# Kernel optimization log

Hardware: AMD Instinct MI355X
Metric: run time of the kernel (lower is better)

## Reference

```python
import jax, jax.numpy as jnp
import numpy as np

HEADS = 16
LN_EPS = 1e-12
MINUS_INF = -10000.0  # matches DeepSpeed's minus_inf constant


def setup_inputs() -> dict:
    key = jax.random.key(0)
    ks = jax.random.split(key, 6)
    B, S, H = 2, 2048, 2048
    x = jax.random.normal(ks[0], (B, S, H), dtype=jnp.float32)
    mask = jnp.zeros((B, 1, 1, S), dtype=jnp.float32)  # additive float mask (no padding)
    qkvw = jax.random.normal(ks[1], (H, 3 * H), dtype=jnp.float32) * 0.02
    qkvb = jax.random.normal(ks[2], (3 * H,), dtype=jnp.float32) * 0.02
    ow = jax.random.normal(ks[3], (H, H), dtype=jnp.float32) * 0.02
    norm_w = jnp.ones((H,), dtype=jnp.float32)
    norm_b = jnp.zeros((H,), dtype=jnp.float32)
    return {"x": x, "mask": mask, "qkvw": qkvw, "qkvb": qkvb, "ow": ow,
            "norm_w": norm_w, "norm_b": norm_b}


def _layernorm(x, g, b):
    mu = jnp.mean(x, axis=-1, keepdims=True)
    var = jnp.mean(jnp.square(x - mu), axis=-1, keepdims=True)
    return (x - mu) * jax.lax.rsqrt(var + LN_EPS) * g + b


def reference(x, mask, qkvw, qkvb, ow, norm_w, norm_b):
    B, S, H = x.shape
    dh = H // HEADS
    # QKVGemmOp: fused layernorm + QKV projection
    inp_norm = _layernorm(x, norm_w, norm_b)                      # [B,S,H]
    qkv = jnp.einsum('bsh,he->bse', inp_norm, qkvw) + qkvb        # [B,S,3H]
    q, k, v = jnp.split(qkv, 3, axis=-1)
    q = q.reshape(B, S, HEADS, dh).transpose(0, 2, 1, 3)          # [B,Hd,S,dh]
    k = k.reshape(B, S, HEADS, dh).transpose(0, 2, 1, 3)
    v = v.reshape(B, S, HEADS, dh).transpose(0, 2, 1, 3)
    # SoftmaxContextOp: kernel scales q and k each by 1/norm_factor,
    # norm_factor = d_head**0.25 (use_mup=False) -> net scale 1/sqrt(d_head)
    scale = 1.0 / jnp.sqrt(jnp.asarray(dh, dtype=x.dtype))
    scores = jnp.einsum('bhqd,bhkd->bhqk', q, k) * scale          # [B,Hd,S,S]
    causal = jnp.tril(jnp.ones((S, S), dtype=bool))
    scores = jnp.where(causal[None, None], scores + mask, MINUS_INF)
    probs = jax.nn.softmax(scores, axis=-1)
    ctx = jnp.einsum('bhqk,bhkd->bhqd', probs, v)                 # [B,Hd,S,dh]
    ctx = ctx.transpose(0, 2, 1, 3).reshape(B, S, H)
    # VectorMatMulOp: output projection (no bias here)
    out = jnp.einsum('bsh,ho->bso', ctx, ow)                      # [B,S,H]
    return (out, k, v, ctx, inp_norm)
```

## Files before the change

### kernel.cpp

```cpp
#include <hip/hip_runtime.h>

typedef short bf16x8 __attribute__((ext_vector_type(8)));
typedef float floatx4 __attribute__((ext_vector_type(4)));

#define MFMA16(a, b, c) __builtin_amdgcn_mfma_f32_16x16x32_bf16((a), (b), (c), 0, 0, 0)

__device__ __forceinline__ unsigned short f2bf(float f) {
    union { float f; unsigned int u; } v; v.f = f;
    unsigned int u = v.u;
    return (unsigned short)((u + 0x7FFFu + ((u >> 16) & 1u)) >> 16);
}

__device__ __forceinline__ void gld_lds16(const void* g, void* l) {
    __builtin_amdgcn_global_load_lds(
        (const __attribute__((address_space(1))) unsigned int*)g,
        (__attribute__((address_space(3))) unsigned int*)l, 16, 0, 0);
}

__global__ __launch_bounds__(256) void ln_kernel(
        const float* __restrict__ x, const float* __restrict__ g,
        const float* __restrict__ be, float* __restrict__ yo,
        unsigned short* __restrict__ yb) {
    int row = blockIdx.x, t = threadIdx.x;
    const float* xr = x + (size_t)row * 2048;
    float4 a = ((const float4*)xr)[2 * t];
    float4 b = ((const float4*)xr)[2 * t + 1];
    float s = a.x + a.y + a.z + a.w + b.x + b.y + b.z + b.w;
    float q = a.x * a.x + a.y * a.y + a.z * a.z + a.w * a.w +
              b.x * b.x + b.y * b.y + b.z * b.z + b.w * b.w;
    for (int m = 1; m < 64; m <<= 1) { s += __shfl_xor(s, m); q += __shfl_xor(q, m); }
    __shared__ float red[8];
    if ((t & 63) == 0) { red[t >> 6] = s; red[4 + (t >> 6)] = q; }
    __syncthreads();
    s = red[0] + red[1] + red[2] + red[3];
    q = red[4] + red[5] + red[6] + red[7];
    float mean = s * (1.0f / 2048.0f);
    float var = q * (1.0f / 2048.0f) - mean * mean;
    float rs = rsqrtf(var + 1e-12f);
    float4 g0 = ((const float4*)g)[2 * t], g1 = ((const float4*)g)[2 * t + 1];
    float4 b0 = ((const float4*)be)[2 * t], b1 = ((const float4*)be)[2 * t + 1];
    float4 y0, y1;
    y0.x = (a.x - mean) * rs * g0.x + b0.x;
    y0.y = (a.y - mean) * rs * g0.y + b0.y;
    y0.z = (a.z - mean) * rs * g0.z + b0.z;
    y0.w = (a.w - mean) * rs * g0.w + b0.w;
    y1.x = (b.x - mean) * rs * g1.x + b1.x;
    y1.y = (b.y - mean) * rs * g1.y + b1.y;
    y1.z = (b.z - mean) * rs * g1.z + b1.z;
    y1.w = (b.w - mean) * rs * g1.w + b1.w;
    float* yr = yo + (size_t)row * 2048;
    ((float4*)yr)[2 * t] = y0;
    ((float4*)yr)[2 * t + 1] = y1;
    union { unsigned short u[8]; uint4 v; } pk;
    pk.u[0] = f2bf(y0.x); pk.u[1] = f2bf(y0.y); pk.u[2] = f2bf(y0.z); pk.u[3] = f2bf(y0.w);
    pk.u[4] = f2bf(y1.x); pk.u[5] = f2bf(y1.y); pk.u[6] = f2bf(y1.z); pk.u[7] = f2bf(y1.w);
    *(uint4*)(yb + (size_t)row * 2048 + t * 8) = pk.v;
}

__global__ __launch_bounds__(256) void transpose_cvt(
        const float* __restrict__ src, unsigned short* __restrict__ dst,
        int K, int N) {
    __shared__ unsigned short tile[64][73];
    int n0 = blockIdx.x * 64, k0 = blockIdx.y * 64;
    size_t bo = (size_t)blockIdx.z * K * N;
    int t = threadIdx.x;
    for (int p = 0; p < 4; p++) {
        int idx = p * 256 + t; int r = idx >> 4; int c = (idx & 15) * 4;
        float4 v = *(const float4*)(src + bo + (size_t)(k0 + r) * N + n0 + c);
        tile[r][c] = f2bf(v.x); tile[r][c + 1] = f2bf(v.y);
        tile[r][c + 2] = f2bf(v.z); tile[r][c + 3] = f2bf(v.w);
    }
    __syncthreads();
    for (int p = 0; p < 4; p++) {
        int idx = p * 256 + t; int n = idx >> 4; int c = (idx & 15) * 4;
        ushort4 o;
        o.x = tile[c][n]; o.y = tile[c + 1][n];
        o.z = tile[c + 2][n]; o.w = tile[c + 3][n];
        *(ushort4*)(dst + bo + (size_t)(n0 + n) * K + k0 + c) = o;
    }
}

#define NT_QKV 32

__device__ __forceinline__ void stage_A(const unsigned short* __restrict__ Ag,
        unsigned short* As, int mh, int m0, int kt, int tid) {
#pragma unroll
    for (int j = 0; j < 2; j++) {
        int G = j * 512 + tid;
        int s = (G >> 3) & 63;
        int gr = G & 7;
        int row = j * 128 + mh * 64 + s;
        const unsigned short* src =
            Ag + (size_t)(m0 + row) * 2048 + kt * 64 + ((gr ^ (s & 7)) << 3);
        unsigned short* dst = As + j * 8192 + mh * 4096 + (tid >> 6) * 512;
        gld_lds16(src, dst);
    }
}

__device__ __forceinline__ void stage_B(const unsigned short* __restrict__ Bg,
        unsigned short* Bs, int nh, int n0, int kt, int tid) {
#pragma unroll
    for (int j = 0; j < 2; j++) {
        int G = j * 512 + tid;
        int wcc = G >> 8;
        int s = (G >> 3) & 31;
        int gr = G & 7;
        int row = wcc * 64 + nh * 32 + s;
        const unsigned short* src =
            Bg + (size_t)(n0 + row) * 2048 + kt * 64 + ((gr ^ (s & 7)) << 3);
        unsigned short* dst = Bs + wcc * 4096 + nh * 2048 + ((tid >> 6) & 3) * 512;
        gld_lds16(src, dst);
    }
}

__device__ __forceinline__ bf16x8 ldfrag(const unsigned short* S, int row, int ks,
                                         int quad, int ln15) {
    int gr = ((ks << 2) | quad) ^ (ln15 & 7);
    return *(const bf16x8*)(S + row * 64 + gr * 8);
}

#define PHASE_SYNC()                                        \
    __builtin_amdgcn_s_barrier();                           \
    asm volatile("s_waitcnt lgkmcnt(0)" ::: "memory");      \
    __builtin_amdgcn_sched_barrier(0);                      \
    __builtin_amdgcn_s_setprio(1)

#define PHASE_END()                                         \
    __builtin_amdgcn_s_setprio(0);                          \
    asm volatile("s_waitcnt vmcnt(4)" ::: "memory");        \
    __builtin_amdgcn_s_barrier()

__device__ __forceinline__ void qkv_tile(
        const unsigned short* __restrict__ Ag, const unsigned short* __restrict__ Bg,
        unsigned short* Asc, unsigned short* Bsc,
        unsigned short* Asn, unsigned short* Bsn,
        int t, int m0, int n0, int tid, int wr, int wc, int ln15, int quad,
        floatx4 (&acc)[8][4]) {
    bf16x8 a[4][2], bb[2][2];
    bool pf = (t + 1 < NT_QKV);
#pragma unroll
    for (int m = 0; m < 4; m++) {
        a[m][0] = ldfrag(Asc, wr * 128 + m * 16 + ln15, 0, quad, ln15);
        a[m][1] = ldfrag(Asc, wr * 128 + m * 16 + ln15, 1, quad, ln15);
    }
#pragma unroll
    for (int n = 0; n < 2; n++) {
        bb[n][0] = ldfrag(Bsc, wc * 64 + n * 16 + ln15, 0, quad, ln15);
        bb[n][1] = ldfrag(Bsc, wc * 64 + n * 16 + ln15, 1, quad, ln15);
    }
    if (pf) stage_B(Bg, Bsn, 0, n0, t + 1, tid);
    PHASE_SYNC();
#pragma unroll
    for (int m = 0; m < 4; m++)
#pragma unroll
        for (int n = 0; n < 2; n++) {
            acc[m][n] = MFMA16(a[m][0], bb[n][0], acc[m][n]);
            acc[m][n] = MFMA16(a[m][1], bb[n][1], acc[m][n]);
        }
    PHASE_END();
#pragma unroll
    for (int n = 0; n < 2; n++) {
        bb[n][0] = ldfrag(Bsc, wc * 64 + (2 + n) * 16 + ln15, 0, quad, ln15);
        bb[n][1] = ldfrag(Bsc, wc * 64 + (2 + n) * 16 + ln15, 1, quad, ln15);
    }
    if (pf) stage_A(Ag, Asn, 0, m0, t + 1, tid);
    PHASE_SYNC();
#pragma unroll
    for (int m = 0; m < 4; m++)
#pragma unroll
        for (int n = 0; n < 2; n++) {
            acc[m][2 + n] = MFMA16(a[m][0], bb[n][0], acc[m][2 + n]);
            acc[m][2 + n] = MFMA16(a[m][1], bb[n][1], acc[m][2 + n]);
        }
    PHASE_END();
#pragma unroll
    for (int m = 0; m < 4; m++) {
        a[m][0] = ldfrag(Asc, wr * 128 + (4 + m) * 16 + ln15, 0, quad, ln15);
        a[m][1] = ldfrag(Asc, wr * 128 + (4 + m) * 16 + ln15, 1, quad, ln15);
    }
    if (pf) stage_B(Bg, Bsn, 1, n0, t + 1, tid);
    PHASE_SYNC();
#pragma unroll
    for (int m = 0; m < 4; m++)
#pragma unroll
        for (int n = 0; n < 2; n++) {
            acc[4 + m][2 + n] = MFMA16(a[m][0], bb[n][0], acc[4 + m][2 + n]);
            acc[4 + m][2 + n] = MFMA16(a[m][1], bb[n][1], acc[4 + m][2 + n]);
        }
    PHASE_END();
#pragma unroll
    for (int n = 0; n < 2; n++) {
        bb[n][0] = ldfrag(Bsc, wc * 64 + n * 16 + ln15, 0, quad, ln15);
        bb[n][1] = ldfrag(Bsc, wc * 64 + n * 16 + ln15, 1, quad, ln15);
    }
    if (pf) stage_A(Ag, Asn, 1, m0, t + 1, tid);
    PHASE_SYNC();
#pragma unroll
    for (int m = 0; m < 4; m++)
#pragma unroll
        for (int n = 0; n < 2; n++) {
            acc[4 + m][n] = MFMA16(a[m][0], bb[n][0], acc[4 + m][n]);
            acc[4 + m][n] = MFMA16(a[m][1], bb[n][1], acc[4 + m][n]);
        }
    PHASE_END();
}

__global__ __launch_bounds__(512, 2) void gemm_qkv(
        const unsigned short* __restrict__ A, const unsigned short* __restrict__ Bt,
        const float* __restrict__ bias, float* __restrict__ ko,
        float* __restrict__ vo, unsigned short* __restrict__ qws,
        unsigned short* __restrict__ kbf) {
    __shared__ __align__(16) unsigned short As[2][16384];
    __shared__ __align__(16) unsigned short Bs[2][16384];
    int bid = blockIdx.x;
    int xcd = bid & 7, idx = bid >> 3;
    int mt = (xcd & 3) * 4 + idx / 12;
    int ntile = (xcd >> 2) * 12 + idx % 12;
    int m0 = mt * 256, n0 = ntile * 256;
    int tid = threadIdx.x;
    int wave = tid >> 6, lane = tid & 63, ln15 = lane & 15, quad = lane >> 4;
    int wr = wave >> 2, wc = wave & 3;
    floatx4 acc[8][4] = {};
    stage_B(Bt, Bs[0], 0, n0, 0, tid);
    stage_A(A, As[0], 0, m0, 0, tid);
    stage_B(Bt, Bs[0], 1, n0, 0, tid);
    stage_A(A, As[0], 1, m0, 0, tid);
    asm volatile("s_waitcnt vmcnt(4)" ::: "memory");
    __builtin_amdgcn_s_barrier();
#pragma unroll 1
    for (int t = 0; t < NT_QKV; t += 2) {
        qkv_tile(A, Bt, As[0], Bs[0], As[1], Bs[1], t,     m0, n0, tid, wr, wc, ln15, quad, acc);
        qkv_tile(A, Bt, As[1], Bs[1], As[0], Bs[0], t + 1, m0, n0, tid, wr, wc, ln15, quad, acc);
    }
#pragma unroll
    for (int mi = 0; mi < 8; mi++) {
        int row = m0 + wr * 128 + mi * 16 + quad * 4;
#pragma unroll
        for (int ni = 0; ni < 4; ni++) {
            int col = n0 + wc * 64 + ni * 16 + ln15;
            float bv = bias[col];
#pragma unroll
            for (int r = 0; r < 4; r++) {
                float val = acc[mi][ni][r] + bv;
                int rr = row + r;
                int b = rr >> 11, s = rr & 2047;
                if (col < 2048) {
                    qws[(size_t)rr * 2048 + col] = f2bf(val);
                } else if (col < 4096) {
                    int cc = col - 2048; int h = cc >> 7, d = cc & 127;
                    size_t o = ((size_t)(b * 16 + h) * 2048 + s) * 128 + d;
                    ko[o] = val;
                    kbf[o] = f2bf(val);
                } else {
                    int cc = col - 4096; int h = cc >> 7, d = cc & 127;
                    vo[((size_t)(b * 16 + h) * 2048 + s) * 128 + d] = val;
                }
            }
        }
    }
}

__global__ __launch_bounds__(256) void gemm_out(
        const float* __restrict__ Actx, const unsigned short* __restrict__ Bt,
        float* __restrict__ out) {
    __shared__ unsigned short As[128 * 72];
    __shared__ unsigned short Bs[128 * 72];
    int m0 = blockIdx.y * 128, n0 = blockIdx.x * 128;
    int t = threadIdx.x;
    int wave = t >> 6, lane = t & 63, ln15 = lane & 15, quad = lane >> 4;
    int wm = wave >> 1, wn = wave & 1;
    floatx4 acc[4][4] = {};
    for (int k0 = 0; k0 < 2048; k0 += 64) {
        for (int p = 0; p < 4; p++) {
            int idx = p * 256 + t; int r = idx >> 3; int c = (idx & 7) * 8;
            const float* ap = Actx + (size_t)(m0 + r) * 2048 + k0 + c;
            float4 u0 = ((const float4*)ap)[0], u1 = ((const float4*)ap)[1];
            union { unsigned short u[8]; uint4 v; } pk;
            pk.u[0] = f2bf(u0.x); pk.u[1] = f2bf(u0.y); pk.u[2] = f2bf(u0.z); pk.u[3] = f2bf(u0.w);
            pk.u[4] = f2bf(u1.x); pk.u[5] = f2bf(u1.y); pk.u[6] = f2bf(u1.z); pk.u[7] = f2bf(u1.w);
            *(uint4*)&As[r * 72 + c] = pk.v;
            *(uint4*)&Bs[r * 72 + c] = *(const uint4*)(Bt + (size_t)(n0 + r) * 2048 + k0 + c);
        }
        __syncthreads();
        for (int ks = 0; ks < 2; ks++) {
            bf16x8 af[4], bfr[4];
            for (int i = 0; i < 4; i++)
                af[i] = *(const bf16x8*)&As[(wm * 64 + i * 16 + ln15) * 72 + ks * 32 + quad * 8];
            for (int i = 0; i < 4; i++)
                bfr[i] = *(const bf16x8*)&Bs[(wn * 64 + i * 16 + ln15) * 72 + ks * 32 + quad * 8];
            for (int mi = 0; mi < 4; mi++)
                for (int ni = 0; ni < 4; ni++)
                    acc[mi][ni] = MFMA16(af[mi], bfr[ni], acc[mi][ni]);
        }
        __syncthreads();
    }
    for (int mi = 0; mi < 4; mi++) {
        int row = m0 + wm * 64 + mi * 16 + quad * 4;
        for (int ni = 0; ni < 4; ni++) {
            int col = n0 + wn * 64 + ni * 16 + ln15;
            for (int r = 0; r < 4; r++)
                out[(size_t)(row + r) * 2048 + col] = acc[mi][ni][r];
        }
    }
}

__device__ __forceinline__ void stage_kv(const unsigned short* __restrict__ kb,
                                         const unsigned short* __restrict__ vTb,
                                         int c0, int tid,
                                         unsigned short* KsB, unsigned short* VtB) {
    int wb = (tid >> 6) << 6;
#pragma unroll
    for (int i = 0; i < 4; i++) {
        int p = i * 256 + tid;
        int r = p >> 4, s = p & 15;
        int g = s ^ (r & 7);
        gld_lds16(kb + (size_t)(c0 + r) * 128 + g * 8, KsB + (i * 256 + wb) * 8);
    }
#pragma unroll
    for (int i = 0; i < 4; i++) {
        int p = i * 256 + tid;
        int d = p >> 3, s = p & 7;
        int g = s ^ (d & 7);
        gld_lds16(vTb + (size_t)d * 2048 + c0 + g * 8, VtB + (i * 256 + wb) * 8);
    }
}

__global__ __launch_bounds__(256, 2) void attn_kernel(
        const unsigned short* __restrict__ qws, const unsigned short* __restrict__ kbf,
        const unsigned short* __restrict__ vT, const float* __restrict__ mask,
        float* __restrict__ ctxo) {
    __shared__ __align__(16) unsigned short Ks[2][64 * 128];
    __shared__ __align__(16) unsigned short Vt[2][128 * 64];
    __shared__ unsigned short Pl[4 * 16 * 72];
    int jp = blockIdx.x, h = blockIdx.y, b = blockIdx.z;
    int t = threadIdx.x, wave = t >> 6, lane = t & 63, ln15 = lane & 15, quad = lane >> 4;
    int x7 = ln15 & 7;
    const float scale = 0.08838834764831845f;

    const unsigned short* kb = kbf + (size_t)(b * 16 + h) * 2048 * 128;
    const unsigned short* vTb = vT + (size_t)(b * 16 + h) * 128 * 2048;
    const float* mb = mask + (size_t)b * 2048;

    int cur = 0;
    stage_kv(kb, vTb, 0, t, Ks[0], Vt[0]);

#pragma unroll 1
    for (int half = 0; half < 2; half++) {
        int qt = half ? (31 - jp) : jp;
        int Q0 = qt * 64;

        bf16x8 qf[4];
        const unsigned short* qbase =
            qws + ((size_t)(b * 2048 + Q0 + wave * 16 + ln15)) * 2048 + h * 128;
#pragma unroll
        for (int ks = 0; ks < 4; ks++)
            qf[ks] = *(const bf16x8*)(qbase + ks * 32 + quad * 8);

        float m_r[4], l_r[4];
        floatx4 o[8] = {};
#pragma unroll
        for (int r = 0; r < 4; r++) { m_r[r] = -1e30f; l_r[r] = 0.0f; }

        int nkt = qt + 1;
#pragma unroll 1
        for (int kt = 0; kt < nkt; kt++) {
            int c0 = kt * 64;
            bool hn = true; int nc0 = 0;
            if (kt + 1 < nkt)      nc0 = c0 + 64;
            else if (half == 0)    nc0 = 0;
            else                   hn = false;
            if (hn) {
                stage_kv(kb, vTb, nc0, t, Ks[cur ^ 1], Vt[cur ^ 1]);
                asm volatile("s_waitcnt vmcnt(8)" ::: "memory");
            } else {
                asm volatile("s_waitcnt vmcnt(0)" ::: "memory");
            }
            __builtin_amdgcn_s_barrier();
            const unsigned short* KsB = Ks[cur];
            const unsigned short* VtB = Vt[cur];

            floatx4 cs[4] = {};
            __builtin_amdgcn_s_setprio(1);
#pragma unroll
            for (int ks = 0; ks < 4; ks++)
#pragma unroll
                for (int ni = 0; ni < 4; ni++) {
                    int rr = ni * 16 + ln15;
                    int sl = (ks * 4 + quad) ^ x7;
                    bf16x8 kfr = *(const bf16x8*)&KsB[rr * 128 + sl * 8];
                    cs[ni] = MFMA16(qf[ks], kfr, cs[ni]);
                }
            __builtin_amdgcn_s_setprio(0);

            float sv[4][4];
            float mt[4] = {-1e30f, -1e30f, -1e30f, -1e30f};
            if (kt == qt) {
#pragma unroll
                for (int ni = 0; ni < 4; ni++) {
                    int cg = c0 + ni * 16 + ln15;
                    float mk = mb[cg];
#pragma unroll
                    for (int r = 0; r < 4; r++) {
                        int qg = Q0 + wave * 16 + quad * 4 + r;
                        float v = (cg <= qg) ? fmaf(cs[ni][r], scale, mk) : -10000.0f;
                        sv[ni][r] = v;
                        mt[r] = fmaxf(mt[r], v);
                    }
                }
            } else {
#pragma unroll
                for (int ni = 0; ni < 4; ni++) {
                    float mk = mb[c0 + ni * 16 + ln15];
#pragma unroll
                    for (int r = 0; r < 4; r++) {
                        float v = fmaf(cs[ni][r], scale, mk);
                        sv[ni][r] = v;
                        mt[r] = fmaxf(mt[r], v);
                    }
                }
            }
#pragma unroll
            for (int m = 1; m < 16; m <<= 1)
#pragma unroll
                for (int r = 0; r < 4; r++) mt[r] = fmaxf(mt[r], __shfl_xor(mt[r], m));

            bool grow = false;
#pragma unroll
            for (int r = 0; r < 4; r++) grow = grow || (mt[r] > m_r[r] + 8.0f);
            if (__any((int)grow)) {
#pragma unroll
                for (int r = 0; r < 4; r++) {
                    float mn = fmaxf(m_r[r], mt[r]);
                    float al = __expf(m_r[r] - mn);
                    m_r[r] = mn;
                    l_r[r] *= al;
#pragma unroll
                    for (int nj = 0; nj < 8; nj++) o[nj][r] *= al;
                }
            }

            float lt[4] = {0.0f, 0.0f, 0.0f, 0.0f};
#pragma unroll
            for (int ni = 0; ni < 4; ni++)
#pragma unroll
                for (int r = 0; r < 4; r++) {
                    float p = __expf(sv[ni][r] - m_r[r]);
                    sv[ni][r] = p;
                    lt[r] += p;
                }
#pragma unroll
            for (int m = 1; m < 16; m <<= 1)
#pragma unroll
                for (int r = 0; r < 4; r++) lt[r] += __shfl_xor(lt[r], m);
#pragma unroll
            for (int r = 0; r < 4; r++) l_r[r] += lt[r];

            unsigned short* pw = &Pl[wave * 16 * 72];
#pragma unroll
            for (int ni = 0; ni < 4; ni++)
#pragma unroll
                for (int r = 0; r < 4; r++)
                    pw[(quad * 4 + r) * 72 + ni * 16 + ln15] = f2bf(sv[ni][r]);

            __builtin_amdgcn_s_setprio(1);
#pragma unroll
            for (int ks2 = 0; ks2 < 2; ks2++) {
                bf16x8 pf = *(const bf16x8*)&Pl[(wave * 16 + ln15) * 72 + ks2 * 32 + quad * 8];
#pragma unroll
                for (int nj = 0; nj < 8; nj++) {
                    int dd = nj * 16 + ln15;
                    int sl = (ks2 * 4 + quad) ^ x7;
                    bf16x8 vf = *(const bf16x8*)&VtB[dd * 64 + sl * 8];
                    o[nj] = MFMA16(pf, vf, o[nj]);
                }
            }
            __builtin_amdgcn_s_setprio(0);
            __builtin_amdgcn_s_barrier();
            cur ^= 1;
        }

        float rl[4];
#pragma unroll
        for (int r = 0; r < 4; r++) rl[r] = 1.0f / l_r[r];
#pragma unroll
        for (int nj = 0; nj < 8; nj++)
#pragma unroll
            for (int r = 0; r < 4; r++) {
                int s = Q0 + wave * 16 + quad * 4 + r;
                ctxo[((size_t)(b * 2048 + s)) * 2048 + h * 128 + nj * 16 + ln15] = o[nj][r] * rl[r];
            }
    }
}

extern "C" void kernel_launch(void* const* d_in, const int* in_sizes, int n_in,
                              void* d_out, int out_size, void* d_ws, size_t ws_size,
                              hipStream_t stream) {
    const float* x      = (const float*)d_in[0];
    const float* mask   = (const float*)d_in[1];
    const float* qkvw   = (const float*)d_in[2];
    const float* qkvb   = (const float*)d_in[3];
    const float* ow     = (const float*)d_in[4];
    const float* norm_w = (const float*)d_in[5];
    const float* norm_b = (const float*)d_in[6];

    float* out      = (float*)d_out;
    float* k_out    = out + 8388608;
    float* v_out    = out + 16777216;
    float* ctx_out  = out + 25165824;
    float* norm_out = out + 33554432;

    unsigned short* ws    = (unsigned short*)d_ws;
    unsigned short* xn    = ws;
    unsigned short* qkvwT = ws + 8388608;
    unsigned short* owT   = ws + 8388608 + 12582912;
    unsigned short* qws   = owT + 4194304;
    unsigned short* vT    = qws + 8388608;
    unsigned short* kbf   = vT + 8388608;

    ln_kernel<<<4096, 256, 0, stream>>>(x, norm_w, norm_b, norm_out, xn);
    transpose_cvt<<<dim3(96, 32, 1), 256, 0, stream>>>(qkvw, qkvwT, 2048, 6144);
    transpose_cvt<<<dim3(32, 32, 1), 256, 0, stream>>>(ow, owT, 2048, 2048);
    gemm_qkv<<<dim3(384), 512, 0, stream>>>(xn, qkvwT, qkvb, k_out, v_out, qws, kbf);
    transpose_cvt<<<dim3(2, 32, 32), 256, 0, stream>>>(v_out, vT, 2048, 128);
    attn_kernel<<<dim3(16, 16, 2), 256, 0, stream>>>(qws, kbf, vT, mask, ctx_out);
    gemm_out<<<dim3(16, 32), 256, 0, stream>>>(ctx_out, owT, out);
}
```

Measured before the change: 550.6 us.

## Fuse prep kernels, emit bf16 ctx from attention, async-load gemm_out tiles

Merges layernorm and both weight transpose-converts into one launch. The attention kernel now also writes a bf16 copy of ctx into the freed xn workspace, so gemm_out no longer reads fp32 ctx and converts it per tile. gemm_out loads A and B straight into LDS with global_load_lds, uses an unpadded 64-stride layout, and remaps blocks for XCD locality. This trades extra bf16 stores in attention and possible LDS bank conflicts from dropping the padding for less conversion work and fewer launches.

After: 542.6 us. Within noise of the previous version (-1.4%).

```diff
diff --git a/kernel.cpp b/kernel.cpp
--- a/kernel.cpp
+++ b/kernel.cpp
@@ -17,44 +17,75 @@
         (__attribute__((address_space(3))) unsigned int*)l, 16, 0, 0);
 }
 
-__global__ __launch_bounds__(256) void ln_kernel(
+__global__ __launch_bounds__(256) void prep_kernel(
         const float* __restrict__ x, const float* __restrict__ g,
         const float* __restrict__ be, float* __restrict__ yo,
-        unsigned short* __restrict__ yb) {
-    int row = blockIdx.x, t = threadIdx.x;
-    const float* xr = x + (size_t)row * 2048;
-    float4 a = ((const float4*)xr)[2 * t];
-    float4 b = ((const float4*)xr)[2 * t + 1];
-    float s = a.x + a.y + a.z + a.w + b.x + b.y + b.z + b.w;
-    float q = a.x * a.x + a.y * a.y + a.z * a.z + a.w * a.w +
-              b.x * b.x + b.y * b.y + b.z * b.z + b.w * b.w;
-    for (int m = 1; m < 64; m <<= 1) { s += __shfl_xor(s, m); q += __shfl_xor(q, m); }
+        unsigned short* __restrict__ yb,
+        const float* __restrict__ qkvw, unsigned short* __restrict__ qkvwT,
+        const float* __restrict__ ow, unsigned short* __restrict__ owT) {
     __shared__ float red[8];
-    if ((t & 63) == 0) { red[t >> 6] = s; red[4 + (t >> 6)] = q; }
+    __shared__ unsigned short tile[64][73];
+    int bid = blockIdx.x, t = threadIdx.x;
+    if (bid < 4096) {
+        int row = bid;
+        const float* xr = x + (size_t)row * 2048;
+        float4 a = ((const float4*)xr)[2 * t];
+        float4 b = ((const float4*)xr)[2 * t + 1];
+        float s = a.x + a.y + a.z + a.w + b.x + b.y + b.z + b.w;
+        float q = a.x * a.x + a.y * a.y + a.z * a.z + a.w * a.w +
+                  b.x * b.x + b.y * b.y + b.z * b.z + b.w * b.w;
+        for (int m = 1; m < 64; m <<= 1) { s += __shfl_xor(s, m); q += __shfl_xor(q, m); }
+        if ((t & 63) == 0) { red[t >> 6] = s; red[4 + (t >> 6)] = q; }
+        __syncthreads();
+        s = red[0] + red[1] + red[2] + red[3];
+        q = red[4] + red[5] + red[6] + red[7];
+        float mean = s * (1.0f / 2048.0f);
+        float var = q * (1.0f / 2048.0f) - mean * mean;
+        float rs = rsqrtf(var + 1e-12f);
+        float4 g0 = ((const float4*)g)[2 * t], g1 = ((const float4*)g)[2 * t + 1];
+        float4 b0 = ((const float4*)be)[2 * t], b1 = ((const float4*)be)[2 * t + 1];
+        float4 y0, y1;
+        y0.x = (a.x - mean) * rs * g0.x + b0.x;
+        y0.y = (a.y - mean) * rs * g0.y + b0.y;
+        y0.z = (a.z - mean) * rs * g0.z + b0.z;
+        y0.w = (a.w - mean) * rs * g0.w + b0.w;
+        y1.x = (b.x - mean) * rs * g1.x + b1.x;
+        y1.y = (b.y - mean) * rs * g1.y + b1.y;
+        y1.z = (b.z - mean) * rs * g1.z + b1.z;
+        y1.w = (b.w - mean) * rs * g1.w + b1.w;
+        float* yr = yo + (size_t)row * 2048;
+        ((float4*)yr)[2 * t] = y0;
+        ((float4*)yr)[2 * t + 1] = y1;
+        union { unsigned short u[8]; uint4 v; } pk;
+        pk.u[0] = f2bf(y0.x); pk.u[1] = f2bf(y0.y); pk.u[2] = f2bf(y0.z); pk.u[3] = f2bf(y0.w);
+        pk.u[4] = f2bf(y1.x); pk.u[5] = f2bf(y1.y); pk.u[6] = f2bf(y1.z); pk.u[7] = f2bf(y1.w);
+        *(uint4*)(yb + (size_t)row * 2048 + t * 8) = pk.v;
+        return;
+    }
+    const float* src; unsigned short* dst; int N, n0, k0;
+    if (bid < 4096 + 3072) {
+        int b2 = bid - 4096;
+        src = qkvw; dst = qkvwT; N = 6144;
+        n0 = (b2 % 96) * 64; k0 = (b2 / 96) * 64;
+    } else {
+        int b3 = bid - 7168;
+        src = ow; dst = owT; N = 2048;
+        n0 = (b3 % 32) * 64; k0 = (b3 / 32) * 64;
+    }
+    for (int p = 0; p < 4; p++) {
+        int idx = p * 256 + t; int r = idx >> 4; int c = (idx & 15) * 4;
+        float4 v = *(const float4*)(src + (size_t)(k0 + r) * N + n0 + c);
+        tile[r][c] = f2bf(v.x); tile[r][c + 1] = f2bf(v.y);
+        tile[r][c + 2] = f2bf(v.z); tile[r][c + 3] = f2bf(v.w);
+    }
     __syncthreads();
-    s = red[0] + red[1] + red[2] + red[3];
-    q = red[4] + red[5] + red[6] + red[7];
-    float mean = s * (1.0f / 2048.0f);
-    float var = q * (1.0f / 2048.0f) - mean * mean;
-    float rs = rsqrtf(var + 1e-12f);
-    float4 g0 = ((const float4*)g)[2 * t], g1 = ((const float4*)g)[2 * t + 1];
-    float4 b0 = ((const float4*)be)[2 * t], b1 = ((const float4*)be)[2 * t + 1];
-    float4 y0, y1;
-    y0.x = (a.x - mean) * rs * g0.x + b0.x;
-    y0.y = (a.y - mean) * rs * g0.y + b0.y;
-    y0.z = (a.z - mean) * rs * g0.z + b0.z;
-    y0.w = (a.w - mean) * rs * g0.w + b0.w;
-    y1.x = (b.x - mean) * rs * g1.x + b1.x;
-    y1.y = (b.y - mean) * rs * g1.y + b1.y;
-    y1.z = (b.z - mean) * rs * g1.z + b1.z;
-    y1.w = (b.w - mean) * rs * g1.w + b1.w;
-    float* yr = yo + (size_t)row * 2048;
-    ((float4*)yr)[2 * t] = y0;
-    ((float4*)yr)[2 * t + 1] = y1;
-    union { unsigned short u[8]; uint4 v; } pk;
-    pk.u[0] = f2bf(y0.x); pk.u[1] = f2bf(y0.y); pk.u[2] = f2bf(y0.z); pk.u[3] = f2bf(y0.w);
-    pk.u[4] = f2bf(y1.x); pk.u[5] = f2bf(y1.y); pk.u[6] = f2bf(y1.z); pk.u[7] = f2bf(y1.w);
-    *(uint4*)(yb + (size_t)row * 2048 + t * 8) = pk.v;
+    for (int p = 0; p < 4; p++) {
+        int idx = p * 256 + t; int n = idx >> 4; int c = (idx & 15) * 4;
+        ushort4 o;
+        o.x = tile[c][n]; o.y = tile[c + 1][n];
+        o.z = tile[c + 2][n]; o.w = tile[c + 3][n];
+        *(ushort4*)(dst + (size_t)(n0 + n) * 2048 + k0 + c) = o;
+    }
 }
 
 __global__ __launch_bounds__(256) void transpose_cvt(
@@ -261,33 +292,32 @@
 }
 
 __global__ __launch_bounds__(256) void gemm_out(
-        const float* __restrict__ Actx, const unsigned short* __restrict__ Bt,
+        const unsigned short* __restrict__ Ab, const unsigned short* __restrict__ Bt,
         float* __restrict__ out) {
-    __shared__ unsigned short As[128 * 72];
-    __shared__ unsigned short Bs[128 * 72];
-    int m0 = blockIdx.y * 128, n0 = blockIdx.x * 128;
+    __shared__ unsigned short As[128 * 64];
+    __shared__ unsigned short Bs[128 * 64];
+    int bid = blockIdx.x;
+    int xcd = bid & 7, idx = bid >> 3;
+    int mt = (xcd & 3) * 8 + (idx >> 3);
+    int nt = (xcd >> 2) * 8 + (idx & 7);
+    int m0 = mt * 128, n0 = nt * 128;
     int t = threadIdx.x;
     int wave = t >> 6, lane = t & 63, ln15 = lane & 15, quad = lane >> 4;
     int wm = wave >> 1, wn = wave & 1;
     floatx4 acc[4][4] = {};
     for (int k0 = 0; k0 < 2048; k0 += 64) {
         for (int p = 0; p < 4; p++) {
-            int idx = p * 256 + t; int r = idx >> 3; int c = (idx & 7) * 8;
-            const float* ap = Actx + (size_t)(m0 + r) * 2048 + k0 + c;
-            float4 u0 = ((const float4*)ap)[0], u1 = ((const float4*)ap)[1];
-            union { unsigned short u[8]; uint4 v; } pk;
-            pk.u[0] = f2bf(u0.x); pk.u[1] = f2bf(u0.y); pk.u[2] = f2bf(u0.z); pk.u[3] = f2bf(u0.w);
-            pk.u[4] = f2bf(u1.x); pk.u[5] = f2bf(u1.y); pk.u[6] = f2bf(u1.z); pk.u[7] = f2bf(u1.w);
-            *(uint4*)&As[r * 72 + c] = pk.v;
-            *(uint4*)&Bs[r * 72 + c] = *(const uint4*)(Bt + (size_t)(n0 + r) * 2048 + k0 + c);
+            int ix = p * 256 + t; int r = ix >> 3; int c = (ix & 7) * 8;
+            gld_lds16(Ab + (size_t)(m0 + r) * 2048 + k0 + c, As + p * 2048 + wave * 512);
+            gld_lds16(Bt + (size_t)(n0 + r) * 2048 + k0 + c, Bs + p * 2048 + wave * 512);
         }
         __syncthreads();
         for (int ks = 0; ks < 2; ks++) {
             bf16x8 af[4], bfr[4];
             for (int i = 0; i < 4; i++)
-                af[i] = *(const bf16x8*)&As[(wm * 64 + i * 16 + ln15) * 72 + ks * 32 + quad * 8];
+                af[i] = *(const bf16x8*)&As[(wm * 64 + i * 16 + ln15) * 64 + ks * 32 + quad * 8];
             for (int i = 0; i < 4; i++)
-                bfr[i] = *(const bf16x8*)&Bs[(wn * 64 + i * 16 + ln15) * 72 + ks * 32 + quad * 8];
+                bfr[i] = *(const bf16x8*)&Bs[(wn * 64 + i * 16 + ln15) * 64 + ks * 32 + quad * 8];
             for (int mi = 0; mi < 4; mi++)
                 for (int ni = 0; ni < 4; ni++)
                     acc[mi][ni] = MFMA16(af[mi], bfr[ni], acc[mi][ni]);
@@ -328,7 +358,7 @@
 __global__ __launch_bounds__(256, 2) void attn_kernel(
         const unsigned short* __restrict__ qws, const unsigned short* __restrict__ kbf,
         const unsigned short* __restrict__ vT, const float* __restrict__ mask,
-        float* __restrict__ ctxo) {
+        float* __restrict__ ctxo, unsigned short* __restrict__ ctxb) {
     __shared__ __align__(16) unsigned short Ks[2][64 * 128];
     __shared__ __align__(16) unsigned short Vt[2][128 * 64];
     __shared__ unsigned short Pl[4 * 16 * 72];
@@ -487,7 +517,10 @@
 #pragma unroll
             for (int r = 0; r < 4; r++) {
                 int s = Q0 + wave * 16 + quad * 4 + r;
-                ctxo[((size_t)(b * 2048 + s)) * 2048 + h * 128 + nj * 16 + ln15] = o[nj][r] * rl[r];
+                size_t off = ((size_t)(b * 2048 + s)) * 2048 + h * 128 + nj * 16 + ln15;
+                float val = o[nj][r] * rl[r];
+                ctxo[off] = val;
+                ctxb[off] = f2bf(val);
             }
     }
 }
@@ -517,11 +550,10 @@
     unsigned short* vT    = qws + 8388608;
     unsigned short* kbf   = vT + 8388608;
 
-    ln_kernel<<<4096, 256, 0, stream>>>(x, norm_w, norm_b, norm_out, xn);
-    transpose_cvt<<<dim3(96, 32, 1), 256, 0, stream>>>(qkvw, qkvwT, 2048, 6144);
-    transpose_cvt<<<dim3(32, 32, 1), 256, 0, stream>>>(ow, owT, 2048, 2048);
+    prep_kernel<<<8192, 256, 0, stream>>>(x, norm_w, norm_b, norm_out, xn,
+                                          qkvw, qkvwT, ow, owT);
     gemm_qkv<<<dim3(384), 512, 0, stream>>>(xn, qkvwT, qkvb, k_out, v_out, qws, kbf);
     transpose_cvt<<<dim3(2, 32, 32), 256, 0, stream>>>(v_out, vT, 2048, 128);
-    attn_kernel<<<dim3(16, 16, 2), 256, 0, stream>>>(qws, kbf, vT, mask, ctx_out);
-    gemm_out<<<dim3(16, 32), 256, 0, stream>>>(ctx_out, owT, out);
-}
+    attn_kernel<<<dim3(16, 16, 2), 256, 0, stream>>>(qws, kbf, vT, mask, ctx_out, xn);
+    gemm_out<<<dim3(512), 256, 0, stream>>>(xn, owT, out);
+}
```
